# Optimization experiments

Measured on AMD Instinct MI355X. Metric: run time of the kernel, lower is better.

## Reference

```python
import jax, jax.numpy as jnp
import numpy as np

N_NODES = 100000
N_EDGES = 400000   # number of hyperedges
N_INC = 1600000    # incidence pairs (node, hyperedge)
N_GRAPHS = 512
ATOM_DIM = 92
NODE_DIM = 64
H_DIM = 128
NUM_LAYERS = 3
BN_EPS = 1e-5


def setup_inputs() -> dict:
    key = jax.random.key(0)
    ks = jax.random.split(key, 10)
    x = jax.random.normal(ks[0], (N_NODES, ATOM_DIM), jnp.float32)
    node_idx = jax.random.randint(ks[1], (N_INC,), 0, N_NODES)
    edge_idx = jax.random.randint(ks[2], (N_INC,), 0, N_EDGES)
    batch = jnp.sort(jax.random.randint(ks[3], (N_NODES,), 0, N_GRAPHS))

    def lin(k, fan_in, shape):
        return jax.random.normal(k, shape, jnp.float32) / np.float32(np.sqrt(fan_in))

    W_emb = lin(ks[4], ATOM_DIM, (ATOM_DIM, NODE_DIM))
    b_emb = jnp.zeros((NODE_DIM,), jnp.float32)
    conv_W = lin(ks[5], NODE_DIM, (NUM_LAYERS, NODE_DIM, NODE_DIM))
    conv_b = jnp.zeros((NUM_LAYERS, NODE_DIM), jnp.float32)
    bn_gamma = jnp.ones((NUM_LAYERS, NODE_DIM), jnp.float32)
    bn_beta = jnp.zeros((NUM_LAYERS, NODE_DIM), jnp.float32)
    fc_W = lin(ks[6], NODE_DIM, (NODE_DIM, H_DIM))
    fc_b = jnp.zeros((H_DIM,), jnp.float32)
    fco_W = lin(ks[7], H_DIM, (H_DIM, 1))
    fco_b = jnp.zeros((1,), jnp.float32)
    return {
        "x": x, "W_emb": W_emb, "b_emb": b_emb,
        "conv_W": conv_W, "conv_b": conv_b,
        "bn_gamma": bn_gamma, "bn_beta": bn_beta,
        "fc_W": fc_W, "fc_b": fc_b, "fco_W": fco_W, "fco_b": fco_b,
        "node_idx": node_idx, "edge_idx": edge_idx, "batch": batch,
    }


def _hypergraph_conv(h, W, b, gamma, beta, node_idx, edge_idx):
    """PyG-style HypergraphConv: X' = D^-1 H B^-1 H^T (X Theta), then BN + softplus."""
    h = h @ W + b  # [N, F]
    ones = jnp.ones((N_INC,), h.dtype)
    deg_e = jax.ops.segment_sum(ones, edge_idx, num_segments=N_EDGES)  # |e| per hyperedge
    Binv = jnp.where(deg_e > 0, 1.0 / deg_e, 0.0)
    # node -> hyperedge: mean of member node features
    e_feat = jax.ops.segment_sum(h[node_idx], edge_idx, num_segments=N_EDGES) * Binv[:, None]
    deg_n = jax.ops.segment_sum(ones, node_idx, num_segments=N_NODES)  # node hyperedge-degree
    Dinv = jnp.where(deg_n > 0, 1.0 / deg_n, 0.0)
    # hyperedge -> node
    out = jax.ops.segment_sum(e_feat[edge_idx], node_idx, num_segments=N_NODES) * Dinv[:, None]
    # BatchNorm1d over node dimension (training-mode batch statistics, biased var)
    mean = out.mean(axis=0)
    var = jnp.mean(jnp.square(out - mean), axis=0)
    out = gamma * (out - mean) * jax.lax.rsqrt(var + BN_EPS) + beta
    return jax.nn.softplus(out)


def reference(x, W_emb, b_emb, conv_W, conv_b, bn_gamma, bn_beta,
              fc_W, fc_b, fco_W, fco_b, node_idx, edge_idx, batch):
    h = x @ W_emb + b_emb  # [N, node_dim]
    for l in range(NUM_LAYERS):
        h = _hypergraph_conv(h, conv_W[l], conv_b[l], bn_gamma[l], bn_beta[l],
                             node_idx, edge_idx)
    # scatter-mean pooling over graphs
    cnt = jax.ops.segment_sum(jnp.ones((N_NODES,), h.dtype), batch, num_segments=N_GRAPHS)
    pooled = jax.ops.segment_sum(h, batch, num_segments=N_GRAPHS) / jnp.maximum(cnt, 1.0)[:, None]
    g = jax.nn.softplus(pooled)
    g = jax.nn.softplus(g @ fc_W + fc_b)
    return g @ fco_W + fco_b  # [N_GRAPHS, 1]
```

## Files before the change

kernel.cpp:

```cpp
#include <hip/hip_runtime.h>
#include <hip/hip_fp16.h>
#include <math.h>

#define N_NODES   100000
#define N_EDGES   400000
#define N_INC     1600000
#define N_GRAPHS  512
#define ATOM_DIM  92
#define NODE_DIM  64
#define H_DIM     128
#define NUM_LAYERS 3
#define BN_EPS    1e-5f

#define NBUCK     391
#define PCHUNK    2048
#define NCHP      ((N_INC + PCHUNK - 1) / PCHUNK)
#define MM_BLOCKS 1568

struct alignas(8)  half4 { __half2 a, b; };
struct alignas(16) half8 { __half2 a, b, c, d; };
typedef __attribute__((ext_vector_type(8))) float float8;
typedef __attribute__((ext_vector_type(2))) float float2v;
typedef __attribute__((ext_vector_type(4))) float f32x4;
typedef _Float16 f16x8 __attribute__((ext_vector_type(8)));

__device__ __forceinline__ float softplus_f(float x) {
    return fmaxf(x, 0.f) + log1pf(expf(-fabsf(x)));
}

__device__ __forceinline__ float8 cvt8(half8 v) {
    float2 p0 = __half22float2(v.a), p1 = __half22float2(v.b);
    float2 p2 = __half22float2(v.c), p3 = __half22float2(v.d);
    float8 r;
    r[0] = p0.x; r[1] = p0.y; r[2] = p1.x; r[3] = p1.y;
    r[4] = p2.x; r[5] = p2.y; r[6] = p3.x; r[7] = p3.y;
    return r;
}
__device__ __forceinline__ half8 cvt16(float8 v) {
    half8 r;
    r.a = __floats2half2_rn(v[0], v[1]);
    r.b = __floats2half2_rn(v[2], v[3]);
    r.c = __floats2half2_rn(v[4], v[5]);
    r.d = __floats2half2_rn(v[6], v[7]);
    return r;
}

__device__ __forceinline__ float8 fp8x8_to_f32u(unsigned lo, unsigned hi) {
    float2v l0 = __builtin_amdgcn_cvt_pk_f32_fp8((int)lo, false);
    float2v h0 = __builtin_amdgcn_cvt_pk_f32_fp8((int)lo, true);
    float2v l1 = __builtin_amdgcn_cvt_pk_f32_fp8((int)hi, false);
    float2v h1 = __builtin_amdgcn_cvt_pk_f32_fp8((int)hi, true);
    float8 r;
    r[0] = l0.x; r[1] = l0.y; r[2] = h0.x; r[3] = h0.y;
    r[4] = l1.x; r[5] = l1.y; r[6] = h1.x; r[7] = h1.y;
    return r;
}
__device__ __forceinline__ float8 fp8x8_to_f32(uint2 v) {
    return fp8x8_to_f32u(v.x, v.y);
}
__device__ __forceinline__ uint2 f32_to_fp8x8(float8 v) {
    int a = 0, b = 0;
    a = __builtin_amdgcn_cvt_pk_fp8_f32(v[0], v[1], a, false);
    a = __builtin_amdgcn_cvt_pk_fp8_f32(v[2], v[3], a, true);
    b = __builtin_amdgcn_cvt_pk_fp8_f32(v[4], v[5], b, false);
    b = __builtin_amdgcn_cvt_pk_fp8_f32(v[6], v[7], b, true);
    uint2 r; r.x = (unsigned)a; r.y = (unsigned)b;
    return r;
}


__global__ void __launch_bounds__(256) embed_mfma(
        const float* __restrict__ x, const float* __restrict__ W,
        const float* __restrict__ bvec, uint2* __restrict__ h8) {
    __shared__ half8 so8[4][16][9];
    int tid = threadIdx.x;
    int w = tid >> 6, lane = tid & 63;
    int l15 = lane & 15, rg = lane >> 4;
    __half* so_h = (__half*)so8[w];

    f16x8 bf[4][3];
    #pragma unroll
    for (int c = 0; c < 4; ++c)
        #pragma unroll
        for (int kk = 0; kk < 3; ++kk)
            #pragma unroll
            for (int j = 0; j < 8; ++j) {
                int k = kk * 32 + rg * 8 + j;
                bf[c][kk][j] = (k < ATOM_DIM) ? (_Float16)W[k * 64 + c * 16 + l15]
                                              : (_Float16)0.f;
            }
    float bias[4];
    #pragma unroll
    for (int c = 0; c < 4; ++c) bias[c] = bvec[c * 16 + l15];

    int wave_global = blockIdx.x * 4 + w;
    for (int tile = wave_global; tile < N_NODES / 16; tile += MM_BLOCKS * 4) {
        int n0 = tile * 16;
        const float* xrow = x + (size_t)(n0 + l15) * ATOM_DIM;
        f16x8 af[3];
        #pragma unroll
        for (int kk = 0; kk < 3; ++kk) {
            int k0 = kk * 32 + rg * 8;
            if (k0 + 8 <= ATOM_DIM) {
                float4 v0 = *(const float4*)&xrow[k0];
                float4 v1 = *(const float4*)&xrow[k0 + 4];
                af[kk][0] = (_Float16)v0.x; af[kk][1] = (_Float16)v0.y;
                af[kk][2] = (_Float16)v0.z; af[kk][3] = (_Float16)v0.w;
                af[kk][4] = (_Float16)v1.x; af[kk][5] = (_Float16)v1.y;
                af[kk][6] = (_Float16)v1.z; af[kk][7] = (_Float16)v1.w;
            } else {
                float4 v0 = *(const float4*)&xrow[88];
                af[kk][0] = (_Float16)v0.x; af[kk][1] = (_Float16)v0.y;
                af[kk][2] = (_Float16)v0.z; af[kk][3] = (_Float16)v0.w;
                af[kk][4] = (_Float16)0.f;  af[kk][5] = (_Float16)0.f;
                af[kk][6] = (_Float16)0.f;  af[kk][7] = (_Float16)0.f;
            }
        }
        #pragma unroll
        for (int c = 0; c < 4; ++c) {
            f32x4 acc = {0.f, 0.f, 0.f, 0.f};
            acc = __builtin_amdgcn_mfma_f32_16x16x32_f16(af[0], bf[c][0], acc, 0, 0, 0);
            acc = __builtin_amdgcn_mfma_f32_16x16x32_f16(af[1], bf[c][1], acc, 0, 0, 0);
            acc = __builtin_amdgcn_mfma_f32_16x16x32_f16(af[2], bf[c][2], acc, 0, 0, 0);
            #pragma unroll
            for (int i = 0; i < 4; ++i)
                so_h[(rg * 4 + i) * 72 + c * 16 + l15] = __float2half_rn(acc[i] + bias[c]);
        }
        #pragma unroll
        for (int it = 0; it < 2; ++it) {
            int row = (lane >> 3) + it * 8;
            half8 v = *(half8*)&so_h[row * 72 + (lane & 7) * 8];
            h8[(size_t)(n0 + row) * 8 + (lane & 7)] = f32_to_fp8x8(cvt8(v));
        }
    }
}


__global__ void __launch_bounds__(256) part_hist_dual(
        const int* __restrict__ ekey, const int* __restrict__ nkey,
        int* __restrict__ histsE, int* __restrict__ histsN) {
    __shared__ int hE[NBUCK];
    __shared__ int hN[NBUCK];
    int tid = threadIdx.x;
    int base = blockIdx.x * PCHUNK;
    for (int i = tid; i < NBUCK; i += 256) { hE[i] = 0; hN[i] = 0; }
    __syncthreads();
    #pragma unroll
    for (int k = 0; k < 8; ++k) {
        int i = base + tid + k * 256;
        if (i < N_INC) {
            atomicAdd(&hE[ekey[i] >> 10], 1);
            atomicAdd(&hN[nkey[i] >> 8], 1);
        }
    }
    __syncthreads();
    for (int i = tid; i < NBUCK; i += 256) {
        histsE[(size_t)blockIdx.x * NBUCK + i] = hE[i];
        histsN[(size_t)blockIdx.x * NBUCK + i] = hN[i];
    }
}

__global__ void __launch_bounds__(256) col_scan_dual(
        int* __restrict__ histsE, int* __restrict__ histsN,
        int* __restrict__ colsumE, int* __restrict__ colsumN) {
    __shared__ int ws[256];
    int which = blockIdx.x >= NBUCK;
    int i = which ? (blockIdx.x - NBUCK) : blockIdx.x;
    int* hists = which ? histsN : histsE;
    int* colsum = which ? colsumN : colsumE;
    int tid = threadIdx.x;
    int v[4];
    int loc = 0;
    #pragma unroll
    for (int k = 0; k < 4; ++k) {
        int b = tid * 4 + k;
        v[k] = (b < NCHP) ? hists[(size_t)b * NBUCK + i] : 0;
        loc += v[k];
    }
    ws[tid] = loc;
    __syncthreads();
    for (int off = 1; off < 256; off <<= 1) {
        int t = (tid >= off) ? ws[tid - off] : 0;
        __syncthreads();
        ws[tid] += t;
        __syncthreads();
    }
    int run = ws[tid] - loc;
    if (tid == 255) colsum[i] = ws[255];
    #pragma unroll
    for (int k = 0; k < 4; ++k) {
        int b = tid * 4 + k;
        if (b < NCHP) hists[(size_t)b * NBUCK + i] = run;
        run += v[k];
    }
}

__global__ void bbase_scan_dual(const int* __restrict__ colsumE, const int* __restrict__ colsumN,
                                int* __restrict__ bbaseE, int* __restrict__ bbaseN) {
    __shared__ int sh[512];
    const int* colsum = blockIdx.x ? colsumN : colsumE;
    int* bbase = blockIdx.x ? bbaseN : bbaseE;
    int tid = threadIdx.x;
    int v = (tid < NBUCK) ? colsum[tid] : 0;
    sh[tid] = v;
    __syncthreads();
    for (int off = 1; off < 512; off <<= 1) {
        int t = (tid >= off) ? sh[tid - off] : 0;
        __syncthreads();
        sh[tid] += t;
        __syncthreads();
    }
    if (tid <= NBUCK)
        bbase[tid] = (tid == 0) ? 0 : sh[tid - 1];
}

__global__ void __launch_bounds__(256) part_scatter_dual(
        const int* __restrict__ ekey, const int* __restrict__ nkey,
        const int* __restrict__ histsE, const int* __restrict__ histsN,
        const int* __restrict__ bbaseE, const int* __restrict__ bbaseN,
        unsigned* __restrict__ stagingE, unsigned* __restrict__ stagingN) {
    __shared__ int curE[NBUCK];
    __shared__ int curN[NBUCK];
    int tid = threadIdx.x;
    int base = blockIdx.x * PCHUNK;
    int kE[8], kN[8];
    #pragma unroll
    for (int k = 0; k < 8; ++k) {
        int i = base + tid + k * 256;
        bool ok = (i < N_INC);
        kE[k] = ok ? ekey[i] : -1;
        kN[k] = ok ? nkey[i] : 0;
    }
    for (int i = tid; i < NBUCK; i += 256) {
        curE[i] = bbaseE[i] + histsE[(size_t)blockIdx.x * NBUCK + i];
        curN[i] = bbaseN[i] + histsN[(size_t)blockIdx.x * NBUCK + i];
    }
    __syncthreads();
    #pragma unroll
    for (int k = 0; k < 8; ++k) {
        if (kE[k] >= 0) {
            int pe = atomicAdd(&curE[kE[k] >> 10], 1);
            stagingE[pe] = ((unsigned)(kE[k] & 1023) << 17) | (unsigned)kN[k];
            int pn = atomicAdd(&curN[kN[k] >> 8], 1);
            stagingN[pn] = ((unsigned)(kN[k] & 255) << 19) | (unsigned)kE[k];
        }
    }
}

template<int RANGE, int PAYBITS>
__device__ void finalize_impl(const unsigned* __restrict__ staging,
                              const int* __restrict__ bbase, int b,
                              int nIds, float* __restrict__ inv,
                              int* __restrict__ off, int* __restrict__ list,
                              int* hist, int* wsum) {
    const int PER = RANGE / 256;
    const unsigned PAYMASK = (1u << PAYBITS) - 1u;
    int tid = threadIdx.x;
    int s = bbase[b], t = bbase[b + 1];
    int id0 = b * RANGE;
    for (int i = tid; i < RANGE; i += 256) hist[i] = 0;
    __syncthreads();
    for (int j = s + tid; j < t; j += 256) {
        unsigned key = staging[j] >> PAYBITS;
        atomicAdd(&hist[key], 1);
    }
    __syncthreads();
    int base0 = tid * PER;
    int vals[PER];
    int local = 0;
    #pragma unroll
    for (int k = 0; k < PER; ++k) { vals[k] = hist[base0 + k]; local += vals[k]; }
    wsum[tid] = local;
    __syncthreads();
    for (int o = 1; o < 256; o <<= 1) {
        int tv = (tid >= o) ? wsum[tid - o] : 0;
        __syncthreads();
        wsum[tid] += tv;
        __syncthreads();
    }
    int run = wsum[tid] - local;
    #pragma unroll
    for (int k = 0; k < PER; ++k) {
        int id = id0 + base0 + k;
        int gpos = s + run;
        if (id < nIds) {
            off[id] = gpos;
            inv[id] = vals[k] > 0 ? 1.f / (float)vals[k] : 0.f;
        } else if (id == nIds) {
            off[nIds] = gpos;
        }
        hist[base0 + k] = gpos;
        run += vals[k];
    }
    __syncthreads();
    for (int j = s + tid; j < t; j += 256) {
        unsigned it = staging[j];
        unsigned key = it >> PAYBITS;
        int pos = atomicAdd(&hist[key], 1);
        list[pos] = (int)(it & PAYMASK);
    }
}

__global__ void __launch_bounds__(256) bucket_finalize_dual(
        const unsigned* __restrict__ stagingE, const unsigned* __restrict__ stagingN,
        const int* __restrict__ bbaseE, const int* __restrict__ bbaseN,
        float* __restrict__ binv, float* __restrict__ dinv,
        int* __restrict__ eoff, int* __restrict__ noff,
        int* __restrict__ elist, int* __restrict__ nlist) {
    __shared__ int hist[1024];
    __shared__ int wsum[256];
    if (blockIdx.x < NBUCK) {
        finalize_impl<1024, 17>(stagingE, bbaseE, blockIdx.x, N_EDGES, binv, eoff, elist,
                                hist, wsum);
    } else {
        finalize_impl<256, 19>(stagingN, bbaseN, blockIdx.x - NBUCK, N_NODES, dinv, noff, nlist,
                               hist, wsum);
    }
}


__global__ void __launch_bounds__(256) edge_agg(
        const int* __restrict__ eoff, const int* __restrict__ elist,
        const uint4* __restrict__ h16B, const float* __restrict__ binv,
        uint4* __restrict__ efeat16B) {
    int e = blockIdx.x * 64 + (threadIdx.x >> 2);
    if (e >= N_EDGES) return;
    int q = threadIdx.x & 3;
    int s = eoff[e], t = eoff[e + 1];
    float8 alo = (float8)0.f, ahi = (float8)0.f;
    float8 blo = (float8)0.f, bhi = (float8)0.f;
    int j = s;
    for (; j + 1 < t; j += 2) {
        int n0 = __ldg(&elist[j]), n1 = __ldg(&elist[j + 1]);
        uint4 v0 = __ldg(&h16B[(size_t)n0 * 4 + q]);
        uint4 v1 = __ldg(&h16B[(size_t)n1 * 4 + q]);
        alo += fp8x8_to_f32u(v0.x, v0.y); ahi += fp8x8_to_f32u(v0.z, v0.w);
        blo += fp8x8_to_f32u(v1.x, v1.y); bhi += fp8x8_to_f32u(v1.z, v1.w);
    }
    if (j < t) {
        uint4 v0 = __ldg(&h16B[(size_t)__ldg(&elist[j]) * 4 + q]);
        alo += fp8x8_to_f32u(v0.x, v0.y); ahi += fp8x8_to_f32u(v0.z, v0.w);
    }
    alo += blo; ahi += bhi;
    float bv = binv[e];
    alo *= bv; ahi *= bv;
    uint2 lo = f32_to_fp8x8(alo), hi = f32_to_fp8x8(ahi);
    uint4 st; st.x = lo.x; st.y = lo.y; st.z = hi.x; st.w = hi.y;
    efeat16B[(size_t)e * 4 + q] = st;
}

__global__ void __launch_bounds__(256) node_agg(
        const int* __restrict__ noff, const int* __restrict__ nlist,
        const uint4* __restrict__ efeat16B, const float* __restrict__ dinv,
        __half* __restrict__ agg16) {
    int n = blockIdx.x * 64 + (threadIdx.x >> 2);
    if (n >= N_NODES) return;
    int q = threadIdx.x & 3;
    int s = noff[n], t = noff[n + 1];
    float8 l0 = (float8)0.f, h0 = (float8)0.f;
    float8 l1 = (float8)0.f, h1 = (float8)0.f;
    float8 l2 = (float8)0.f, h2 = (float8)0.f;
    float8 l3 = (float8)0.f, h3 = (float8)0.f;
    int j = s;
    for (; j + 3 < t; j += 4) {
        int e0 = __ldg(&nlist[j]),     e1 = __ldg(&nlist[j + 1]);
        int e2 = __ldg(&nlist[j + 2]), e3 = __ldg(&nlist[j + 3]);
        uint4 v0 = __ldg(&efeat16B[(size_t)e0 * 4 + q]);
        uint4 v1 = __ldg(&efeat16B[(size_t)e1 * 4 + q]);
        uint4 v2 = __ldg(&efeat16B[(size_t)e2 * 4 + q]);
        uint4 v3 = __ldg(&efeat16B[(size_t)e3 * 4 + q]);
        l0 += fp8x8_to_f32u(v0.x, v0.y); h0 += fp8x8_to_f32u(v0.z, v0.w);
        l1 += fp8x8_to_f32u(v1.x, v1.y); h1 += fp8x8_to_f32u(v1.z, v1.w);
        l2 += fp8x8_to_f32u(v2.x, v2.y); h2 += fp8x8_to_f32u(v2.z, v2.w);
        l3 += fp8x8_to_f32u(v3.x, v3.y); h3 += fp8x8_to_f32u(v3.z, v3.w);
    }
    for (; j < t; ++j) {
        uint4 v0 = __ldg(&efeat16B[(size_t)__ldg(&nlist[j]) * 4 + q]);
        l0 += fp8x8_to_f32u(v0.x, v0.y); h0 += fp8x8_to_f32u(v0.z, v0.w);
    }
    l0 += l1; l2 += l3; l0 += l2;
    h0 += h1; h2 += h3; h0 += h2;
    float dv = dinv[n];
    l0 *= dv; h0 *= dv;
    *(half8*)&agg16[(size_t)n * 64 + q * 16]     = cvt16(l0);
    *(half8*)&agg16[(size_t)n * 64 + q * 16 + 8] = cvt16(h0);
}


__global__ void __launch_bounds__(256) gemm_bn_kernel(
        const __half* __restrict__ agg16, const float* __restrict__ dinv,
        const float* __restrict__ W, const float* __restrict__ bvec,
        __half* __restrict__ outr16, float* __restrict__ partials) {
    __shared__ half8 so8[4][16][9];
    __shared__ float sred[4][128];
    int tid = threadIdx.x;
    int w = tid >> 6, lane = tid & 63;
    int l15 = lane & 15, rg = lane >> 4;
    __half* so_h = (__half*)so8[w];

    f16x8 bf[4][2];
    #pragma unroll
    for (int c = 0; c < 4; ++c)
        #pragma unroll
        for (int kk = 0; kk < 2; ++kk)
            #pragma unroll
            for (int j = 0; j < 8; ++j) {
                int k = kk * 32 + rg * 8 + j;
                bf[c][kk][j] = (_Float16)W[k * 64 + c * 16 + l15];
            }
    float bias[4];
    #pragma unroll
    for (int c = 0; c < 4; ++c) bias[c] = bvec[c * 16 + l15];

    float sa[4] = {0.f, 0.f, 0.f, 0.f}, sb[4] = {0.f, 0.f, 0.f, 0.f};
    int wave_global = blockIdx.x * 4 + w;
    for (int tile = wave_global; tile < N_NODES / 16; tile += MM_BLOCKS * 4) {
        int n0 = tile * 16;
        f16x8 a0 = *(const f16x8*)&agg16[(size_t)(n0 + l15) * 64 + rg * 8];
        f16x8 a1 = *(const f16x8*)&agg16[(size_t)(n0 + l15) * 64 + 32 + rg * 8];
        float dv[4];
        #pragma unroll
        for (int i = 0; i < 4; ++i) dv[i] = dinv[n0 + rg * 4 + i];
        #pragma unroll
        for (int c = 0; c < 4; ++c) {
            f32x4 acc = {0.f, 0.f, 0.f, 0.f};
            acc = __builtin_amdgcn_mfma_f32_16x16x32_f16(a0, bf[c][0], acc, 0, 0, 0);
            acc = __builtin_amdgcn_mfma_f32_16x16x32_f16(a1, bf[c][1], acc, 0, 0, 0);
            #pragma unroll
            for (int i = 0; i < 4; ++i) {
                float vv = (dv[i] > 0.f) ? (acc[i] + bias[c]) : 0.f;
                sa[c] += vv; sb[c] += vv * vv;
                so_h[(rg * 4 + i) * 72 + c * 16 + l15] = __float2half_rn(vv);
            }
        }
        #pragma unroll
        for (int it = 0; it < 2; ++it) {
            int row = (lane >> 3) + it * 8;
            half8 v = *(half8*)&so_h[row * 72 + (lane & 7) * 8];
            *(half8*)&outr16[(size_t)(n0 + row) * 64 + (lane & 7) * 8] = v;
        }
    }
    #pragma unroll
    for (int c = 0; c < 4; ++c) {
        sa[c] += __shfl_xor(sa[c], 16); sa[c] += __shfl_xor(sa[c], 32);
        sb[c] += __shfl_xor(sb[c], 16); sb[c] += __shfl_xor(sb[c], 32);
    }
    if (rg == 0) {
        #pragma unroll
        for (int c = 0; c < 4; ++c) {
            sred[w][c * 16 + l15]      = sa[c];
            sred[w][64 + c * 16 + l15] = sb[c];
        }
    }
    __syncthreads();
    if (tid < 128) {
        float v = sred[0][tid] + sred[1][tid] + sred[2][tid] + sred[3][tid];
        partials[(size_t)blockIdx.x * 128 + tid] = v;
    }
}


__global__ void __launch_bounds__(256) reduce_bnfin(
        const float* __restrict__ partials, const float* __restrict__ gamma,
        const float* __restrict__ beta, float* __restrict__ scsh) {
    __shared__ float ra[256];
    __shared__ float rb[256];
    int f = blockIdx.x, tid = threadIdx.x;
    float a = 0.f, b = 0.f;
    for (int j = tid; j < MM_BLOCKS; j += 256) {
        a += partials[(size_t)j * 128 + f];
        b += partials[(size_t)j * 128 + 64 + f];
    }
    ra[tid] = a; rb[tid] = b;
    __syncthreads();
    for (int s = 128; s > 0; s >>= 1) {
        if (tid < s) { ra[tid] += ra[tid + s]; rb[tid] += rb[tid + s]; }
        __syncthreads();
    }
    if (tid == 0) {
        const float invN = 1.f / (float)N_NODES;
        float mean = ra[0] * invN;
        float var  = rb[0] * invN - mean * mean;
        var = fmaxf(var, 0.f);
        float sc = gamma[f] * rsqrtf(var + BN_EPS);
        scsh[f]      = sc;
        scsh[64 + f] = beta[f] - mean * sc;
    }
}


__global__ void apply_kernel(const half8* __restrict__ outr8, const float* __restrict__ scsh,
                             uint2* __restrict__ h8) {
    int gid = blockIdx.x * 256 + threadIdx.x;
    if (gid >= N_NODES * 8) return;
    int qq = gid & 7;
    float8 v = cvt8(outr8[gid]);
    float4 sc0 = ((const float4*)scsh)[qq * 2];
    float4 sc1 = ((const float4*)scsh)[qq * 2 + 1];
    float4 sh0 = ((const float4*)(scsh + 64))[qq * 2];
    float4 sh1 = ((const float4*)(scsh + 64))[qq * 2 + 1];
    float8 r;
    r[0] = softplus_f(fmaf(v[0], sc0.x, sh0.x));
    r[1] = softplus_f(fmaf(v[1], sc0.y, sh0.y));
    r[2] = softplus_f(fmaf(v[2], sc0.z, sh0.z));
    r[3] = softplus_f(fmaf(v[3], sc0.w, sh0.w));
    r[4] = softplus_f(fmaf(v[4], sc1.x, sh1.x));
    r[5] = softplus_f(fmaf(v[5], sc1.y, sh1.y));
    r[6] = softplus_f(fmaf(v[6], sc1.z, sh1.z));
    r[7] = softplus_f(fmaf(v[7], sc1.w, sh1.w));
    h8[gid] = f32_to_fp8x8(r);
}


__global__ void pool_head_kernel(const uint2* __restrict__ h8, const int* __restrict__ batch,
                                 const float* __restrict__ fcW, const float* __restrict__ fcb,
                                 const float* __restrict__ fcoW, const float* __restrict__ fcob,
                                 float* __restrict__ out) {
    __shared__ float8 part[32][8];
    __shared__ float p[64];
    __shared__ float red[128];
    __shared__ int seg[2];
    int g = blockIdx.x, tid = threadIdx.x;
    if (tid < 2) {
        int target = g + tid;
        int lo = 0, hi = N_NODES;
        while (lo < hi) {
            int mid = (lo + hi) >> 1;
            if (batch[mid] < target) lo = mid + 1; else hi = mid;
        }
        seg[tid] = lo;
    }
    __syncthreads();
    int s = seg[0], t = seg[1];
    int r = tid >> 3, q = tid & 7;
    float8 acc = (float8)0.f;
    for (int n = s + r; n < t; n += 32)
        acc += fp8x8_to_f32(__ldg(&h8[(size_t)n * 8 + q]));
    part[r][q] = acc;
    __syncthreads();
    for (int st = 16; st >= 1; st >>= 1) {
        if (r < st) part[r][q] += part[r + st][q];
        __syncthreads();
    }
    if (tid < 8) {
        float c = fmaxf((float)(t - s), 1.f);
        float8 v = part[0][tid];
        #pragma unroll
        for (int jj = 0; jj < 8; ++jj)
            p[tid * 8 + jj] = softplus_f(v[jj] / c);
    }
    __syncthreads();
    if (tid < 128) {
        float a = fcb[tid];
        #pragma unroll
        for (int k = 0; k < 64; ++k)
            a = fmaf(p[k], fcW[k * H_DIM + tid], a);
        red[tid] = softplus_f(a) * fcoW[tid];
    }
    __syncthreads();
    for (int st = 64; st > 0; st >>= 1) {
        if (tid < st) red[tid] += red[tid + st];
        __syncthreads();
    }
    if (tid == 0) out[g] = red[0] + fcob[0];
}


extern "C" void kernel_launch(void* const* d_in, const int* in_sizes, int n_in,
                              void* d_out, int out_size, void* d_ws, size_t ws_size,
                              hipStream_t stream) {
    const float* x      = (const float*)d_in[0];
    const float* W_emb  = (const float*)d_in[1];
    const float* b_emb  = (const float*)d_in[2];
    const float* conv_W = (const float*)d_in[3];
    const float* conv_b = (const float*)d_in[4];
    const float* bn_g   = (const float*)d_in[5];
    const float* bn_b   = (const float*)d_in[6];
    const float* fc_W   = (const float*)d_in[7];
    const float* fc_b   = (const float*)d_in[8];
    const float* fco_W  = (const float*)d_in[9];
    const float* fco_b  = (const float*)d_in[10];
    const int* node_idx = (const int*)d_in[11];
    const int* edge_idx = (const int*)d_in[12];
    const int* batch    = (const int*)d_in[13];
    float* out = (float*)d_out;

    uint2*  h8      = (uint2*)d_ws;
    __half* outr16  = (__half*)(h8 + (size_t)N_NODES * 8);
    __half* agg16   = outr16 + (size_t)N_NODES * 64;
    uint2*  efeat8  = (uint2*)(agg16 + (size_t)N_NODES * 64);
    unsigned* stagingE = (unsigned*)(efeat8 + (size_t)N_EDGES * 8);
    unsigned* stagingN = stagingE + N_INC;
    float* binv    = (float*)(stagingN + N_INC);
    float* dinv    = binv   + N_EDGES;
    float* scsh    = dinv   + N_NODES;
    float* partials= scsh   + 128;
    int*   eoff    = (int*)(partials + (size_t)MM_BLOCKS * 128);
    int*   noff    = eoff  + N_EDGES + 1;
    int*   histsE  = noff  + N_NODES + 1;
    int*   histsN  = histsE + (size_t)NCHP * NBUCK;
    int*   colsumE = histsN + (size_t)NCHP * NBUCK;
    int*   colsumN = colsumE + NBUCK;
    int*   bbaseE  = colsumN + NBUCK;
    int*   bbaseN  = bbaseE + NBUCK + 1;
    int*   elist   = bbaseN + NBUCK + 1;
    int*   nlist   = elist + N_INC;

    part_hist_dual<<<NCHP, 256, 0, stream>>>(edge_idx, node_idx, histsE, histsN);
    col_scan_dual<<<2 * NBUCK, 256, 0, stream>>>(histsE, histsN, colsumE, colsumN);
    bbase_scan_dual<<<2, 512, 0, stream>>>(colsumE, colsumN, bbaseE, bbaseN);
    part_scatter_dual<<<NCHP, 256, 0, stream>>>(edge_idx, node_idx, histsE, histsN,
                                                bbaseE, bbaseN, stagingE, stagingN);
    bucket_finalize_dual<<<2 * NBUCK, 256, 0, stream>>>(stagingE, stagingN, bbaseE, bbaseN,
                                                        binv, dinv, eoff, noff, elist, nlist);

    embed_mfma<<<MM_BLOCKS, 256, 0, stream>>>(x, W_emb, b_emb, h8);

    for (int l = 0; l < NUM_LAYERS; ++l) {
        const float* Wl = conv_W + (size_t)l * NODE_DIM * NODE_DIM;
        const float* bl = conv_b + (size_t)l * NODE_DIM;

        edge_agg<<<(N_EDGES + 63) / 64, 256, 0, stream>>>(eoff, elist, (const uint4*)h8,
                                                          binv, (uint4*)efeat8);
        node_agg<<<(N_NODES + 63) / 64, 256, 0, stream>>>(noff, nlist, (const uint4*)efeat8,
                                                          dinv, agg16);
        gemm_bn_kernel<<<MM_BLOCKS, 256, 0, stream>>>(agg16, dinv, Wl, bl, outr16, partials);
        reduce_bnfin<<<64, 256, 0, stream>>>(partials, bn_g + (size_t)l * 64,
                                             bn_b + (size_t)l * 64, scsh);
        apply_kernel<<<(N_NODES * 8 + 255) / 256, 256, 0, stream>>>((const half8*)outr16, scsh, h8);
    }

    pool_head_kernel<<<N_GRAPHS, 256, 0, stream>>>(h8, batch, fc_W, fc_b, fco_W, fco_b, out);
}
```

Measured before the change: 410.5 us.

## Fuse node aggregation into GEMM+BN kernel via shared-memory tile

Merges the node_agg gather kernel with the per-node GEMM/BN-statistics kernel. Each block gathers 64 nodes' hyperedge features into a shared tile, then runs the MFMA matmul on it directly. This removes the fp16 agg buffer round trip through global memory and one launch per layer. In exchange each block now reloads the weights for only 64 nodes, the gather unroll drops from 4 to 2, and reduce_bnfin has many more partial rows (about 1563) to sum.

New measurement: 397.8 us. 3.1% less time.

```diff
diff --git a/kernel.cpp b/kernel.cpp
--- a/kernel.cpp
+++ b/kernel.cpp
@@ -16,6 +16,7 @@
 #define PCHUNK    2048
 #define NCHP      ((N_INC + PCHUNK - 1) / PCHUNK)
 #define MM_BLOCKS 1568
+#define NG_BLOCKS ((N_NODES + 63) / 64)
 
 struct alignas(8)  half4 { __half2 a, b; };
 struct alignas(16) half8 { __half2 a, b, c, d; };
@@ -349,51 +350,45 @@
     efeat16B[(size_t)e * 4 + q] = st;
 }
 
-__global__ void __launch_bounds__(256) node_agg(
+
+__global__ void __launch_bounds__(256) node_gemm_kernel(
         const int* __restrict__ noff, const int* __restrict__ nlist,
         const uint4* __restrict__ efeat16B, const float* __restrict__ dinv,
-        __half* __restrict__ agg16) {
-    int n = blockIdx.x * 64 + (threadIdx.x >> 2);
-    if (n >= N_NODES) return;
-    int q = threadIdx.x & 3;
-    int s = noff[n], t = noff[n + 1];
-    float8 l0 = (float8)0.f, h0 = (float8)0.f;
-    float8 l1 = (float8)0.f, h1 = (float8)0.f;
-    float8 l2 = (float8)0.f, h2 = (float8)0.f;
-    float8 l3 = (float8)0.f, h3 = (float8)0.f;
-    int j = s;
-    for (; j + 3 < t; j += 4) {
-        int e0 = __ldg(&nlist[j]),     e1 = __ldg(&nlist[j + 1]);
-        int e2 = __ldg(&nlist[j + 2]), e3 = __ldg(&nlist[j + 3]);
-        uint4 v0 = __ldg(&efeat16B[(size_t)e0 * 4 + q]);
-        uint4 v1 = __ldg(&efeat16B[(size_t)e1 * 4 + q]);
-        uint4 v2 = __ldg(&efeat16B[(size_t)e2 * 4 + q]);
-        uint4 v3 = __ldg(&efeat16B[(size_t)e3 * 4 + q]);
-        l0 += fp8x8_to_f32u(v0.x, v0.y); h0 += fp8x8_to_f32u(v0.z, v0.w);
-        l1 += fp8x8_to_f32u(v1.x, v1.y); h1 += fp8x8_to_f32u(v1.z, v1.w);
-        l2 += fp8x8_to_f32u(v2.x, v2.y); h2 += fp8x8_to_f32u(v2.z, v2.w);
-        l3 += fp8x8_to_f32u(v3.x, v3.y); h3 += fp8x8_to_f32u(v3.z, v3.w);
-    }
-    for (; j < t; ++j) {
-        uint4 v0 = __ldg(&efeat16B[(size_t)__ldg(&nlist[j]) * 4 + q]);
-        l0 += fp8x8_to_f32u(v0.x, v0.y); h0 += fp8x8_to_f32u(v0.z, v0.w);
-    }
-    l0 += l1; l2 += l3; l0 += l2;
-    h0 += h1; h2 += h3; h0 += h2;
-    float dv = dinv[n];
-    l0 *= dv; h0 *= dv;
-    *(half8*)&agg16[(size_t)n * 64 + q * 16]     = cvt16(l0);
-    *(half8*)&agg16[(size_t)n * 64 + q * 16 + 8] = cvt16(h0);
-}
-
-
-__global__ void __launch_bounds__(256) gemm_bn_kernel(
-        const __half* __restrict__ agg16, const float* __restrict__ dinv,
         const float* __restrict__ W, const float* __restrict__ bvec,
         __half* __restrict__ outr16, float* __restrict__ partials) {
+    __shared__ __half aggT[64][72];
     __shared__ half8 so8[4][16][9];
     __shared__ float sred[4][128];
     int tid = threadIdx.x;
+
+    {
+        int nn = tid >> 2, q = tid & 3;
+        int n = blockIdx.x * 64 + nn;
+        float8 l0 = (float8)0.f, h0 = (float8)0.f;
+        if (n < N_NODES) {
+            int s = noff[n], t = noff[n + 1];
+            float8 l1 = (float8)0.f, h1 = (float8)0.f;
+            int j = s;
+            for (; j + 1 < t; j += 2) {
+                int e0 = __ldg(&nlist[j]), e1 = __ldg(&nlist[j + 1]);
+                uint4 v0 = __ldg(&efeat16B[(size_t)e0 * 4 + q]);
+                uint4 v1 = __ldg(&efeat16B[(size_t)e1 * 4 + q]);
+                l0 += fp8x8_to_f32u(v0.x, v0.y); h0 += fp8x8_to_f32u(v0.z, v0.w);
+                l1 += fp8x8_to_f32u(v1.x, v1.y); h1 += fp8x8_to_f32u(v1.z, v1.w);
+            }
+            if (j < t) {
+                uint4 v0 = __ldg(&efeat16B[(size_t)__ldg(&nlist[j]) * 4 + q]);
+                l0 += fp8x8_to_f32u(v0.x, v0.y); h0 += fp8x8_to_f32u(v0.z, v0.w);
+            }
+            l0 += l1; h0 += h1;
+            float dv = dinv[n];
+            l0 *= dv; h0 *= dv;
+        }
+        *(half8*)&aggT[nn][q * 16]     = cvt16(l0);
+        *(half8*)&aggT[nn][q * 16 + 8] = cvt16(h0);
+    }
+    __syncthreads();
+
     int w = tid >> 6, lane = tid & 63;
     int l15 = lane & 15, rg = lane >> 4;
     __half* so_h = (__half*)so8[w];
@@ -412,30 +407,34 @@
     #pragma unroll
     for (int c = 0; c < 4; ++c) bias[c] = bvec[c * 16 + l15];
 
-    float sa[4] = {0.f, 0.f, 0.f, 0.f}, sb[4] = {0.f, 0.f, 0.f, 0.f};
-    int wave_global = blockIdx.x * 4 + w;
-    for (int tile = wave_global; tile < N_NODES / 16; tile += MM_BLOCKS * 4) {
-        int n0 = tile * 16;
-        f16x8 a0 = *(const f16x8*)&agg16[(size_t)(n0 + l15) * 64 + rg * 8];
-        f16x8 a1 = *(const f16x8*)&agg16[(size_t)(n0 + l15) * 64 + 32 + rg * 8];
-        float dv[4];
-        #pragma unroll
-        for (int i = 0; i < 4; ++i) dv[i] = dinv[n0 + rg * 4 + i];
-        #pragma unroll
-        for (int c = 0; c < 4; ++c) {
-            f32x4 acc = {0.f, 0.f, 0.f, 0.f};
-            acc = __builtin_amdgcn_mfma_f32_16x16x32_f16(a0, bf[c][0], acc, 0, 0, 0);
-            acc = __builtin_amdgcn_mfma_f32_16x16x32_f16(a1, bf[c][1], acc, 0, 0, 0);
-            #pragma unroll
-            for (int i = 0; i < 4; ++i) {
-                float vv = (dv[i] > 0.f) ? (acc[i] + bias[c]) : 0.f;
-                sa[c] += vv; sb[c] += vv * vv;
-                so_h[(rg * 4 + i) * 72 + c * 16 + l15] = __float2half_rn(vv);
-            }
-        }
-        #pragma unroll
-        for (int it = 0; it < 2; ++it) {
-            int row = (lane >> 3) + it * 8;
+    int n0 = blockIdx.x * 64 + w * 16;
+    f16x8 a0 = *(const f16x8*)&aggT[w * 16 + l15][rg * 8];
+    f16x8 a1 = *(const f16x8*)&aggT[w * 16 + l15][32 + rg * 8];
+    float dv[4];
+    #pragma unroll
+    for (int i = 0; i < 4; ++i) {
+        int nr = n0 + rg * 4 + i;
+        dv[i] = (nr < N_NODES) ? dinv[nr] : 0.f;
+    }
+    float sa[4], sb[4];
+    #pragma unroll
+    for (int c = 0; c < 4; ++c) {
+        f32x4 acc = {0.f, 0.f, 0.f, 0.f};
+        acc = __builtin_amdgcn_mfma_f32_16x16x32_f16(a0, bf[c][0], acc, 0, 0, 0);
+        acc = __builtin_amdgcn_mfma_f32_16x16x32_f16(a1, bf[c][1], acc, 0, 0, 0);
+        float va = 0.f, vb = 0.f;
+        #pragma unroll
+        for (int i = 0; i < 4; ++i) {
+            float vv = (dv[i] > 0.f) ? (acc[i] + bias[c]) : 0.f;
+            va += vv; vb += vv * vv;
+            so_h[(rg * 4 + i) * 72 + c * 16 + l15] = __float2half_rn(vv);
+        }
+        sa[c] = va; sb[c] = vb;
+    }
+    #pragma unroll
+    for (int it = 0; it < 2; ++it) {
+        int row = (lane >> 3) + it * 8;
+        if (n0 + row < N_NODES) {
             half8 v = *(half8*)&so_h[row * 72 + (lane & 7) * 8];
             *(half8*)&outr16[(size_t)(n0 + row) * 64 + (lane & 7) * 8] = v;
         }
@@ -467,7 +466,7 @@
     __shared__ float rb[256];
     int f = blockIdx.x, tid = threadIdx.x;
     float a = 0.f, b = 0.f;
-    for (int j = tid; j < MM_BLOCKS; j += 256) {
+    for (int j = tid; j < NG_BLOCKS; j += 256) {
         a += partials[(size_t)j * 128 + f];
         b += partials[(size_t)j * 128 + 64 + f];
     }
@@ -587,15 +586,14 @@
 
     uint2*  h8      = (uint2*)d_ws;
     __half* outr16  = (__half*)(h8 + (size_t)N_NODES * 8);
-    __half* agg16   = outr16 + (size_t)N_NODES * 64;
-    uint2*  efeat8  = (uint2*)(agg16 + (size_t)N_NODES * 64);
+    uint2*  efeat8  = (uint2*)(outr16 + (size_t)N_NODES * 64);
     unsigned* stagingE = (unsigned*)(efeat8 + (size_t)N_EDGES * 8);
     unsigned* stagingN = stagingE + N_INC;
     float* binv    = (float*)(stagingN + N_INC);
     float* dinv    = binv   + N_EDGES;
     float* scsh    = dinv   + N_NODES;
     float* partials= scsh   + 128;
-    int*   eoff    = (int*)(partials + (size_t)MM_BLOCKS * 128);
+    int*   eoff    = (int*)(partials + (size_t)NG_BLOCKS * 128);
     int*   noff    = eoff  + N_EDGES + 1;
     int*   histsE  = noff  + N_NODES + 1;
     int*   histsN  = histsE + (size_t)NCHP * NBUCK;
@@ -622,9 +620,8 @@
 
         edge_agg<<<(N_EDGES + 63) / 64, 256, 0, stream>>>(eoff, elist, (const uint4*)h8,
                                                           binv, (uint4*)efeat8);
-        node_agg<<<(N_NODES + 63) / 64, 256, 0, stream>>>(noff, nlist, (const uint4*)efeat8,
-                                                          dinv, agg16);
-        gemm_bn_kernel<<<MM_BLOCKS, 256, 0, stream>>>(agg16, dinv, Wl, bl, outr16, partials);
+        node_gemm_kernel<<<NG_BLOCKS, 256, 0, stream>>>(noff, nlist, (const uint4*)efeat8,
+                                                        dinv, Wl, bl, outr16, partials);
         reduce_bnfin<<<64, 256, 0, stream>>>(partials, bn_g + (size_t)l * 64,
                                              bn_b + (size_t)l * 64, scsh);
         apply_kernel<<<(N_NODES * 8 + 255) / 256, 256, 0, stream>>>((const half8*)outr16, scsh, h8);
```
